# Kernel optimization log

Measured on AMD Instinct MI355X. Metric: run time of the kernel, lower is better.

Reference implementation:

```python
import jax, jax.numpy as jnp
import numpy as np

B, C_IN, C_OUT, N, K = 32, 128, 128, 128, 3


def setup_inputs() -> dict:
    key = jax.random.key(0)
    k1, k2 = jax.random.split(key)
    # input image batch [B, C_in, N, N]
    x = jax.random.normal(k1, (B, C_IN, N, N), dtype=jnp.float32)
    # learned kernel, matches torch.rand init: [C_out, C_in, K, K]
    kernel = jax.random.uniform(k2, (C_OUT, C_IN, K, K), dtype=jnp.float32)
    return {"x": x, "kernel": kernel}


def reference(x, kernel):
    # BlockConv's banded block-sparse BCSR matmul is mathematically a
    # SAME-zero-padded 2D cross-correlation (no kernel flip):
    #   out[b,o,i,p] = sum_{c,k,d} kernel[o,c,k,d] * x[b,c,i+k-K//2,p+d-K//2]
    # (border blocks in _apply_constraint truncate the kernel exactly like
    #  zero padding). bias=False, so no bias term.
    return jax.lax.conv_general_dilated(
        x, kernel,
        window_strides=(1, 1),
        padding="SAME",
        dimension_numbers=("NCHW", "OIHW", "NCHW"),
    )
```

## Files before the change

kernel.cpp:

```cpp
#include <hip/hip_runtime.h>
#include <hip/hip_bf16.h>

#define B_    32
#define CIN   128
#define COUT  128
#define NN    128
#define PPAD  130
#define ROWE  (PPAD * CIN)
#define XCH   8192
#define ACH   512

typedef __attribute__((ext_vector_type(8))) short short8;
typedef __attribute__((ext_vector_type(4))) float float4v;

static __device__ inline unsigned short f2bf(float f) {
    union { float f; unsigned u; } v; v.f = f;
    unsigned u = v.u;
    unsigned r = u + 0x7FFFu + ((u >> 16) & 1u);
    return (unsigned short)(r >> 16);
}

static __device__ inline void gll16(const unsigned short* g, unsigned short* l) {
    __builtin_amdgcn_global_load_lds((const __attribute__((address_space(1))) unsigned int*)g,
                                     (__attribute__((address_space(3))) unsigned int*)l,
                                     16, 0, 0);
}

__global__ __launch_bounds__(256) void xpose_kernel(const float* __restrict__ x,
                                                    unsigned short* __restrict__ xT) {
    int b = blockIdx.x >> 7;
    int i = blockIdx.x & 127;
    __shared__ unsigned short tile[CIN * PPAD];
    int tid = threadIdx.x;
    const float* src = x + ((size_t)(b * CIN) * NN + i) * NN;
    #pragma unroll
    for (int e = 0; e < 64; ++e) {
        int idx = e * 256 + tid;
        int c = idx >> 7;
        int p = idx & 127;
        tile[c * PPAD + p] = f2bf(src[(size_t)c * (NN * NN) + p]);
    }
    __syncthreads();
    unsigned short* dst = xT + (size_t)(b * NN + i) * ROWE;
    #pragma unroll
    for (int e = 0; e < 32; ++e) {
        int pi = e * 256 + tid;
        int c2 = (pi & 63) * 2;
        int p  = pi >> 6;
        ushort2 v;
        v.x = tile[c2 * PPAD + p];
        v.y = tile[(c2 + 1) * PPAD + p];
        int pp = p + 1;
        int sl = (c2 >> 3) ^ (pp & 15);
        *(ushort2*)(dst + (size_t)pp * CIN + sl * 8 + (c2 & 7)) = v;
    }
    if (tid < 128) {
        dst[tid] = 0;
        dst[(size_t)129 * CIN + tid] = 0;
    }
}

__global__ __launch_bounds__(256) void ktrans_kernel(const float* __restrict__ kern,
                                                     unsigned short* __restrict__ kT2) {
    int idx = blockIdx.x * 256 + threadIdx.x;
    if (idx >= COUT * CIN * 9) return;
    int c  = idx & 127;
    int o  = (idx >> 7) & 127;
    int kd = idx >> 14;
    int k = kd / 3, d = kd % 3;
    float v = kern[(((size_t)o * CIN + c) * 3 + k) * 3 + d];
    kT2[((size_t)(kd * 16 + (c >> 3)) * 128 + o) * 8 + (c & 7)] = f2bf(v);
}

__global__ __launch_bounds__(512, 1) void conv_mfma8_kernel(const unsigned short* __restrict__ xT,
                                                            const unsigned short* __restrict__ kT2,
                                                            float* __restrict__ out) {
    __shared__ unsigned short xs[(XCH + 3 * ACH) * 8];

    int wg = blockIdx.x;
    int lb = (wg & 7) * 256 + (wg >> 3);
    int b  = lb >> 6;
    int rp = lb & 63;

    int tid  = threadIdx.x;
    int lane = tid & 63;
    int wave = tid >> 6;
    int wo = wave >> 2;
    int wr = (wave >> 1) & 1;
    int wq = wave & 1;
    int ob  = wo * 64;
    int pb  = wq * 64;
    int l15 = lane & 15;
    int lg  = lane >> 4;

    {
        const unsigned short* xrow_base = xT + (size_t)b * NN * ROWE;
        #pragma unroll
        for (int s = 0; s < 16; ++s) {
            int W   = s * 512 + tid;
            int r   = W >> 11;
            int rem = W & 2047;
            int grow = rp * 2 - 1 + r;
            int growc = grow < 0 ? 0 : (grow > NN - 1 ? NN - 1 : grow);
            gll16(xrow_base + (size_t)growc * ROWE + (size_t)(rem + 16) * 8,
                  xs + (size_t)W * 8);
        }
        gll16(kT2 + (size_t)tid * 8,         xs + (size_t)(XCH + tid) * 8);
        gll16(kT2 + (size_t)(ACH + tid) * 8, xs + (size_t)(XCH + ACH + tid) * 8);
    }
    asm volatile("s_waitcnt vmcnt(1)" ::: "memory");
    __builtin_amdgcn_s_barrier();

    if (rp == 0) {
        for (int W = tid; W < 2048; W += 512)
            *(short8*)(xs + (size_t)W * 8) = (short8)(0);
    }
    if (rp == 63) {
        for (int W = 3 * 2048 + tid; W < 4 * 2048; W += 512)
            *(short8*)(xs + (size_t)W * 8) = (short8)(0);
    }
    if (rp == 0 || rp == 63) {
        asm volatile("s_waitcnt lgkmcnt(0)" ::: "memory");
        __builtin_amdgcn_s_barrier();
    }

    float4v acc[4][4];
    #pragma unroll
    for (int m = 0; m < 4; ++m)
        #pragma unroll
        for (int n = 0; n < 4; ++n)
            acc[m][n] = (float4v)(0.0f);

    #pragma unroll
    for (int kd = 0; kd < 9; ++kd) {
        const int k = kd / 3, d = kd % 3;
        #pragma unroll
        for (int cc = 0; cc < 4; ++cc) {
            const int ph = kd * 4 + cc;
            short8 a[4], bt[4];
            const unsigned short* ab = xs + (size_t)(XCH + (ph % 3) * ACH) * 8;
            #pragma unroll
            for (int m = 0; m < 4; ++m)
                a[m] = *(const short8*)(ab + ((size_t)lg * 128 + ob + m * 16 + l15) * 8);
            const unsigned short* srow = xs + (size_t)(wr + k) * 2048 * 8;
            #pragma unroll
            for (int n = 0; n < 4; ++n) {
                int q  = pb + n * 16 + l15 + d - 1;
                int qc = q < 0 ? 0 : (q > 127 ? 127 : q);
                int j  = (cc * 4 + lg) ^ ((qc + 1) & 15);
                short8 v = *(const short8*)(srow + ((size_t)qc * 16 + j) * 8);
                bt[n] = (q < 0 || q > 127) ? (short8)(0) : v;
            }
            {
                const int pn = (ph + 2 > 35) ? 35 : (ph + 2);
                gll16(kT2 + ((size_t)pn * ACH + tid) * 8,
                      xs + (size_t)(XCH + (pn % 3) * ACH + tid) * 8);
            }
            __builtin_amdgcn_s_setprio(1);
            #pragma unroll
            for (int m = 0; m < 4; ++m)
                #pragma unroll
                for (int n = 0; n < 4; ++n)
                    acc[m][n] = __builtin_amdgcn_mfma_f32_16x16x32_bf16(a[m], bt[n], acc[m][n], 0, 0, 0);
            __builtin_amdgcn_s_setprio(0);
            asm volatile("s_waitcnt vmcnt(1)" ::: "memory");
            __builtin_amdgcn_s_barrier();
        }
    }

    int row = rp * 2 + wr;
    float* op = out + (size_t)b * COUT * NN * NN + (size_t)row * NN;
    #pragma unroll
    for (int m = 0; m < 4; ++m) {
        #pragma unroll
        for (int n = 0; n < 4; ++n) {
            int p = pb + n * 16 + l15;
            #pragma unroll
            for (int r = 0; r < 4; ++r) {
                int o = ob + m * 16 + lg * 4 + r;
                op[(size_t)o * (NN * NN) + p] = acc[m][n][r];
            }
        }
    }
}

__global__ __launch_bounds__(256) void conv_naive_kernel(const float* __restrict__ x,
                                                         const float* __restrict__ kern,
                                                         float* __restrict__ out) {
    size_t idx = (size_t)blockIdx.x * 256 + threadIdx.x;
    int p = idx & 127;
    size_t t = idx >> 7;
    int i = t & 127; t >>= 7;
    int o = t & 127;
    int b = (int)(t >> 7);
    float s = 0.f;
    for (int c = 0; c < CIN; ++c) {
        #pragma unroll
        for (int k = 0; k < 3; ++k) {
            int r = i + k - 1;
            if (r < 0 || r >= NN) continue;
            #pragma unroll
            for (int d = 0; d < 3; ++d) {
                int q = p + d - 1;
                if (q < 0 || q >= NN) continue;
                s += kern[(((size_t)o * CIN + c) * 3 + k) * 3 + d]
                   * x[(((size_t)b * CIN + c) * NN + r) * NN + q];
            }
        }
    }
    out[idx] = s;
}

extern "C" void kernel_launch(void* const* d_in, const int* in_sizes, int n_in,
                              void* d_out, int out_size, void* d_ws, size_t ws_size,
                              hipStream_t stream) {
    const float* x    = (const float*)d_in[0];
    const float* kern = (const float*)d_in[1];
    float* out = (float*)d_out;

    const size_t xT_bytes  = (size_t)B_ * NN * ROWE * 2;
    const size_t kT_bytes  = (size_t)9 * 16 * 128 * 8 * 2;

    if (ws_size >= xT_bytes + kT_bytes) {
        unsigned short* xT  = (unsigned short*)d_ws;
        unsigned short* kT2 = (unsigned short*)((char*)d_ws + xT_bytes);
        hipLaunchKernelGGL(xpose_kernel, dim3(B_ * NN), dim3(256), 0, stream, x, xT);
        hipLaunchKernelGGL(ktrans_kernel, dim3(576), dim3(256), 0, stream, kern, kT2);
        hipLaunchKernelGGL(conv_mfma8_kernel, dim3(2048), dim3(512), 0, stream, xT, kT2, out);
    } else {
        hipLaunchKernelGGL(conv_naive_kernel, dim3(67108864 / 256), dim3(256), 0, stream,
                           x, kern, out);
    }
}
```

Measured before the change: 258.9 us.

## Double-buffer LDS operand reads in registers and deepen weight prefetch ring

Flattens the kd/cc loops into a single 36-phase loop that loads the A and B operands for the next phase into a second register set while the current phase's MFMAs run. The weight staging ring grows from three to four LDS slots, so global-to-LDS prefetch runs three phases ahead instead of two. The aim is to hide LDS read latency and global load latency behind MFMA work. In exchange it adds 16 operand VGPRs and raises LDS use to the full 160KB per CU.

```diff
diff --git a/kernel.cpp b/kernel.cpp
--- a/kernel.cpp
+++ b/kernel.cpp
@@ -72,10 +72,10 @@
     kT2[((size_t)(kd * 16 + (c >> 3)) * 128 + o) * 8 + (c & 7)] = f2bf(v);
 }
 
-__global__ __launch_bounds__(512, 1) void conv_mfma8_kernel(const unsigned short* __restrict__ xT,
+__global__ __launch_bounds__(512, 1) void conv_mfma9_kernel(const unsigned short* __restrict__ xT,
                                                             const unsigned short* __restrict__ kT2,
                                                             float* __restrict__ out) {
-    __shared__ unsigned short xs[(XCH + 3 * ACH) * 8];
+    __shared__ unsigned short xs[(XCH + 4 * ACH) * 8];
 
     int wg = blockIdx.x;
     int lb = (wg & 7) * 256 + (wg >> 3);
@@ -105,8 +105,9 @@
             gll16(xrow_base + (size_t)growc * ROWE + (size_t)(rem + 16) * 8,
                   xs + (size_t)W * 8);
         }
-        gll16(kT2 + (size_t)tid * 8,         xs + (size_t)(XCH + tid) * 8);
-        gll16(kT2 + (size_t)(ACH + tid) * 8, xs + (size_t)(XCH + ACH + tid) * 8);
+        gll16(kT2 + (size_t)tid * 8,             xs + (size_t)(XCH + tid) * 8);
+        gll16(kT2 + (size_t)(ACH + tid) * 8,     xs + (size_t)(XCH + ACH + tid) * 8);
+        gll16(kT2 + (size_t)(2 * ACH + tid) * 8, xs + (size_t)(XCH + 2 * ACH + tid) * 8);
     }
     asm volatile("s_waitcnt vmcnt(1)" ::: "memory");
     __builtin_amdgcn_s_barrier();
@@ -131,41 +132,59 @@
         for (int n = 0; n < 4; ++n)
             acc[m][n] = (float4v)(0.0f);
 
-    #pragma unroll
-    for (int kd = 0; kd < 9; ++kd) {
-        const int k = kd / 3, d = kd % 3;
-        #pragma unroll
-        for (int cc = 0; cc < 4; ++cc) {
-            const int ph = kd * 4 + cc;
-            short8 a[4], bt[4];
-            const unsigned short* ab = xs + (size_t)(XCH + (ph % 3) * ACH) * 8;
+    short8 aR[2][4], bR[2][4];
+
+    {
+        const unsigned short* ab = xs + (size_t)XCH * 8;
+        #pragma unroll
+        for (int m = 0; m < 4; ++m)
+            aR[0][m] = *(const short8*)(ab + ((size_t)lg * 128 + ob + m * 16 + l15) * 8);
+        const unsigned short* srow = xs + (size_t)wr * 2048 * 8;
+        #pragma unroll
+        for (int n = 0; n < 4; ++n) {
+            int qq = pb + n * 16 + l15 - 1;
+            int qc = qq < 0 ? 0 : (qq > 127 ? 127 : qq);
+            int j  = lg ^ ((qc + 1) & 15);
+            short8 v = *(const short8*)(srow + ((size_t)qc * 16 + j) * 8);
+            bR[0][n] = (qq < 0) ? (short8)(0) : v;
+        }
+    }
+
+    #pragma unroll
+    for (int ph = 0; ph < 36; ++ph) {
+        const int q = ph & 1;
+        {
+            const int pn = (ph + 3 > 35) ? 35 : ph + 3;
+            gll16(kT2 + ((size_t)pn * ACH + tid) * 8,
+                  xs + (size_t)(XCH + (pn & 3) * ACH + tid) * 8);
+        }
+        if (ph < 35) {
+            const int p1  = ph + 1;
+            const int kd1 = p1 >> 2, cc1 = p1 & 3;
+            const int k1  = kd1 / 3, d1 = kd1 % 3;
+            const unsigned short* ab = xs + (size_t)(XCH + (p1 & 3) * ACH) * 8;
             #pragma unroll
             for (int m = 0; m < 4; ++m)
-                a[m] = *(const short8*)(ab + ((size_t)lg * 128 + ob + m * 16 + l15) * 8);
-            const unsigned short* srow = xs + (size_t)(wr + k) * 2048 * 8;
+                aR[q ^ 1][m] = *(const short8*)(ab + ((size_t)lg * 128 + ob + m * 16 + l15) * 8);
+            const unsigned short* srow = xs + (size_t)(wr + k1) * 2048 * 8;
             #pragma unroll
             for (int n = 0; n < 4; ++n) {
-                int q  = pb + n * 16 + l15 + d - 1;
-                int qc = q < 0 ? 0 : (q > 127 ? 127 : q);
-                int j  = (cc * 4 + lg) ^ ((qc + 1) & 15);
+                int qq = pb + n * 16 + l15 + d1 - 1;
+                int qc = qq < 0 ? 0 : (qq > 127 ? 127 : qq);
+                int j  = (cc1 * 4 + lg) ^ ((qc + 1) & 15);
                 short8 v = *(const short8*)(srow + ((size_t)qc * 16 + j) * 8);
-                bt[n] = (q < 0 || q > 127) ? (short8)(0) : v;
+                bR[q ^ 1][n] = (qq < 0 || qq > 127) ? (short8)(0) : v;
             }
-            {
-                const int pn = (ph + 2 > 35) ? 35 : (ph + 2);
-                gll16(kT2 + ((size_t)pn * ACH + tid) * 8,
-                      xs + (size_t)(XCH + (pn % 3) * ACH + tid) * 8);
-            }
-            __builtin_amdgcn_s_setprio(1);
-            #pragma unroll
-            for (int m = 0; m < 4; ++m)
-                #pragma unroll
-                for (int n = 0; n < 4; ++n)
-                    acc[m][n] = __builtin_amdgcn_mfma_f32_16x16x32_bf16(a[m], bt[n], acc[m][n], 0, 0, 0);
-            __builtin_amdgcn_s_setprio(0);
-            asm volatile("s_waitcnt vmcnt(1)" ::: "memory");
-            __builtin_amdgcn_s_barrier();
-        }
+        }
+        __builtin_amdgcn_s_setprio(1);
+        #pragma unroll
+        for (int m = 0; m < 4; ++m)
+            #pragma unroll
+            for (int n = 0; n < 4; ++n)
+                acc[m][n] = __builtin_amdgcn_mfma_f32_16x16x32_bf16(aR[q][m], bR[q][n], acc[m][n], 0, 0, 0);
+        __builtin_amdgcn_s_setprio(0);
+        asm volatile("s_waitcnt vmcnt(1)" ::: "memory");
+        __builtin_amdgcn_s_barrier();
     }
 
     int row = rp * 2 + wr;
@@ -226,7 +245,7 @@
         unsigned short* kT2 = (unsigned short*)((char*)d_ws + xT_bytes);
         hipLaunchKernelGGL(xpose_kernel, dim3(B_ * NN), dim3(256), 0, stream, x, xT);
         hipLaunchKernelGGL(ktrans_kernel, dim3(576), dim3(256), 0, stream, kern, kT2);
-        hipLaunchKernelGGL(conv_mfma8_kernel, dim3(2048), dim3(512), 0, stream, xT, kT2, out);
+        hipLaunchKernelGGL(conv_mfma9_kernel, dim3(2048), dim3(512), 0, stream, xT, kT2, out);
     } else {
         hipLaunchKernelGGL(conv_naive_kernel, dim3(67108864 / 256), dim3(256), 0, stream,
                            x, kern, out);
```

Result: no change. 255.3 us (-1.4%).

## Use 4-wave workgroups with 128x64 per-wave tiles and double-buffered weight slabs

Applied to the files above, without the earlier changes.

The conv kernel drops from 8 waves to 4 per workgroup. Each wave now computes all 128 output channels for a 64-pixel half row, doubling its accumulators to 8x4 MFMA tiles so each B-fragment read from LDS is reused twice as often. Weights stream through two larger 1024-entry slabs (64 input channels per step) instead of three 512-entry slabs, cutting barriers per workgroup from 36 to 18. The cost is higher register pressure, half as many waves to hide latency, and a full vmcnt(0) wait at every step, which serializes the weight prefetch against compute.

```diff
diff --git a/kernel.cpp b/kernel.cpp
--- a/kernel.cpp
+++ b/kernel.cpp
@@ -8,7 +8,7 @@
 #define PPAD  130
 #define ROWE  (PPAD * CIN)
 #define XCH   8192
-#define ACH   512
+#define ASL   1024
 
 typedef __attribute__((ext_vector_type(8))) short short8;
 typedef __attribute__((ext_vector_type(4))) float float4v;
@@ -72,10 +72,11 @@
     kT2[((size_t)(kd * 16 + (c >> 3)) * 128 + o) * 8 + (c & 7)] = f2bf(v);
 }
 
-__global__ __launch_bounds__(512, 1) void conv_mfma8_kernel(const unsigned short* __restrict__ xT,
-                                                            const unsigned short* __restrict__ kT2,
-                                                            float* __restrict__ out) {
-    __shared__ unsigned short xs[(XCH + 3 * ACH) * 8];
+__global__ __launch_bounds__(256, 1) void conv_mfma15_kernel(
+        const unsigned short* __restrict__ xT,
+        const unsigned short* __restrict__ kT2,
+        float* __restrict__ out) {
+    __shared__ unsigned short xs[(XCH + 2 * ASL) * 8];
 
     int wg = blockIdx.x;
     int lb = (wg & 7) * 256 + (wg >> 3);
@@ -85,19 +86,17 @@
     int tid  = threadIdx.x;
     int lane = tid & 63;
     int wave = tid >> 6;
-    int wo = wave >> 2;
-    int wr = (wave >> 1) & 1;
-    int wq = wave & 1;
-    int ob  = wo * 64;
-    int pb  = wq * 64;
+    int wr = wave >> 1;
+    int wp = wave & 1;
+    int pb  = wp * 64;
     int l15 = lane & 15;
     int lg  = lane >> 4;
 
     {
         const unsigned short* xrow_base = xT + (size_t)b * NN * ROWE;
         #pragma unroll
-        for (int s = 0; s < 16; ++s) {
-            int W   = s * 512 + tid;
+        for (int s = 0; s < 32; ++s) {
+            int W   = s * 256 + tid;
             int r   = W >> 11;
             int rem = W & 2047;
             int grow = rp * 2 - 1 + r;
@@ -105,18 +104,21 @@
             gll16(xrow_base + (size_t)growc * ROWE + (size_t)(rem + 16) * 8,
                   xs + (size_t)W * 8);
         }
-        gll16(kT2 + (size_t)tid * 8,         xs + (size_t)(XCH + tid) * 8);
-        gll16(kT2 + (size_t)(ACH + tid) * 8, xs + (size_t)(XCH + ACH + tid) * 8);
-    }
-    asm volatile("s_waitcnt vmcnt(1)" ::: "memory");
+        #pragma unroll
+        for (int s = 0; s < 4; ++s) {
+            int W = s * 256 + tid;
+            gll16(kT2 + (size_t)W * 8, xs + (size_t)(XCH + W) * 8);
+        }
+    }
+    asm volatile("s_waitcnt vmcnt(0)" ::: "memory");
     __builtin_amdgcn_s_barrier();
 
     if (rp == 0) {
-        for (int W = tid; W < 2048; W += 512)
+        for (int W = tid; W < 2048; W += 256)
             *(short8*)(xs + (size_t)W * 8) = (short8)(0);
     }
     if (rp == 63) {
-        for (int W = 3 * 2048 + tid; W < 4 * 2048; W += 512)
+        for (int W = 3 * 2048 + tid; W < 4 * 2048; W += 256)
             *(short8*)(xs + (size_t)W * 8) = (short8)(0);
     }
     if (rp == 0 || rp == 63) {
@@ -124,60 +126,69 @@
         __builtin_amdgcn_s_barrier();
     }
 
-    float4v acc[4][4];
-    #pragma unroll
-    for (int m = 0; m < 4; ++m)
+    float4v acc[8][4];
+    #pragma unroll
+    for (int m = 0; m < 8; ++m)
         #pragma unroll
         for (int n = 0; n < 4; ++n)
             acc[m][n] = (float4v)(0.0f);
 
     #pragma unroll
-    for (int kd = 0; kd < 9; ++kd) {
-        const int k = kd / 3, d = kd % 3;
-        #pragma unroll
-        for (int cc = 0; cc < 4; ++cc) {
-            const int ph = kd * 4 + cc;
-            short8 a[4], bt[4];
-            const unsigned short* ab = xs + (size_t)(XCH + (ph % 3) * ACH) * 8;
+    for (int k = 0; k < 3; ++k) {
+        #pragma unroll
+        for (int d = 0; d < 3; ++d) {
             #pragma unroll
-            for (int m = 0; m < 4; ++m)
-                a[m] = *(const short8*)(ab + ((size_t)lg * 128 + ob + m * 16 + l15) * 8);
-            const unsigned short* srow = xs + (size_t)(wr + k) * 2048 * 8;
-            #pragma unroll
-            for (int n = 0; n < 4; ++n) {
-                int q  = pb + n * 16 + l15 + d - 1;
-                int qc = q < 0 ? 0 : (q > 127 ? 127 : q);
-                int j  = (cc * 4 + lg) ^ ((qc + 1) & 15);
-                short8 v = *(const short8*)(srow + ((size_t)qc * 16 + j) * 8);
-                bt[n] = (q < 0 || q > 127) ? (short8)(0) : v;
+            for (int h = 0; h < 2; ++h) {
+                const int sl = (k * 3 + d) * 2 + h;
+                if (sl < 17) {
+                    const int sn  = sl + 1;
+                    const int kdn = sn >> 1, hn = sn & 1;
+                    #pragma unroll
+                    for (int s = 0; s < 4; ++s) {
+                        int W = s * 256 + tid;
+                        gll16(kT2 + ((size_t)(kdn * 16 + hn * 8) * 128 + W) * 8,
+                              xs + (size_t)(XCH + (sn & 1) * ASL + W) * 8);
+                    }
+                }
+                const unsigned short* ab   = xs + (size_t)(XCH + (sl & 1) * ASL) * 8;
+                const unsigned short* srow = xs + (size_t)(wr + k) * 2048 * 8;
+                #pragma unroll
+                for (int c2 = 0; c2 < 2; ++c2) {
+                    short8 a[8], bt[4];
+                    #pragma unroll
+                    for (int m = 0; m < 8; ++m)
+                        a[m] = *(const short8*)(ab +
+                            ((size_t)((c2 * 4 + lg) * 128) + m * 16 + l15) * 8);
+                    #pragma unroll
+                    for (int n = 0; n < 4; ++n) {
+                        int qq = pb + n * 16 + l15 + d - 1;
+                        int qc = qq < 0 ? 0 : (qq > 127 ? 127 : qq);
+                        int j  = (h * 8 + c2 * 4 + lg) ^ ((qc + 1) & 15);
+                        short8 v = *(const short8*)(srow + ((size_t)qc * 16 + j) * 8);
+                        bt[n] = (qq < 0 || qq > 127) ? (short8)(0) : v;
+                    }
+                    #pragma unroll
+                    for (int m = 0; m < 8; ++m)
+                        #pragma unroll
+                        for (int n = 0; n < 4; ++n)
+                            acc[m][n] = __builtin_amdgcn_mfma_f32_16x16x32_bf16(a[m], bt[n], acc[m][n], 0, 0, 0);
+                }
+                asm volatile("s_waitcnt vmcnt(0)" ::: "memory");
+                __builtin_amdgcn_s_barrier();
             }
-            {
-                const int pn = (ph + 2 > 35) ? 35 : (ph + 2);
-                gll16(kT2 + ((size_t)pn * ACH + tid) * 8,
-                      xs + (size_t)(XCH + (pn % 3) * ACH + tid) * 8);
-            }
-            __builtin_amdgcn_s_setprio(1);
-            #pragma unroll
-            for (int m = 0; m < 4; ++m)
-                #pragma unroll
-                for (int n = 0; n < 4; ++n)
-                    acc[m][n] = __builtin_amdgcn_mfma_f32_16x16x32_bf16(a[m], bt[n], acc[m][n], 0, 0, 0);
-            __builtin_amdgcn_s_setprio(0);
-            asm volatile("s_waitcnt vmcnt(1)" ::: "memory");
-            __builtin_amdgcn_s_barrier();
         }
     }
 
     int row = rp * 2 + wr;
     float* op = out + (size_t)b * COUT * NN * NN + (size_t)row * NN;
     #pragma unroll
-    for (int m = 0; m < 4; ++m) {
+    for (int m = 0; m < 8; ++m) {
         #pragma unroll
         for (int n = 0; n < 4; ++n) {
             int p = pb + n * 16 + l15;
             #pragma unroll
             for (int r = 0; r < 4; ++r) {
-                int o = ob + m * 16 + lg * 4 + r;
+                int o = m * 16 + lg * 4 + r;
                 op[(size_t)o * (NN * NN) + p] = acc[m][n][r];
             }
         }
@@ -201,10 +212,10 @@
             if (r < 0 || r >= NN) continue;
             #pragma unroll
             for (int d = 0; d < 3; ++d) {
-                int q = p + d - 1;
-                if (q < 0 || q >= NN) continue;
+                int qq = p + d - 1;
+                if (qq < 0 || qq >= NN) continue;
                 s += kern[(((size_t)o * CIN + c) * 3 + k) * 3 + d]
-                   * x[(((size_t)b * CIN + c) * NN + r) * NN + q];
+                   * x[(((size_t)b * CIN + c) * NN + r) * NN + qq];
             }
         }
     }
@@ -226,7 +237,7 @@
         unsigned short* kT2 = (unsigned short*)((char*)d_ws + xT_bytes);
         hipLaunchKernelGGL(xpose_kernel, dim3(B_ * NN), dim3(256), 0, stream, x, xT);
         hipLaunchKernelGGL(ktrans_kernel, dim3(576), dim3(256), 0, stream, kern, kT2);
-        hipLaunchKernelGGL(conv_mfma8_kernel, dim3(2048), dim3(512), 0, stream, xT, kT2, out);
+        hipLaunchKernelGGL(conv_mfma15_kernel, dim3(2048), dim3(256), 0, stream, xT, kT2, out);
     } else {
         hipLaunchKernelGGL(conv_naive_kernel, dim3(67108864 / 256), dim3(256), 0, stream,
                            x, kern, out);
```

Measured after the change: 256.3 us. Within noise of the previous version (-1.0%).
